# Kernel optimization log

Measured on AMD Instinct MI355X. Metric: run time of the kernel, lower is better.

Reference implementation:

```python
import jax, jax.numpy as jnp
import numpy as np

SIG = 10.0
C = 0.0
STD = 1.0
N_ATOMS = 21
DESC = N_ATOMS * (N_ATOMS - 1) // 2  # 210
N_TRAIN = 4096
M = 128


def setup_inputs() -> dict:
    key = jax.random.key(0)
    k1, k2, k3 = jax.random.split(key, 3)
    # Cartesian coordinates, spread out so interatomic distances are O(1)
    Rs = jax.random.normal(k1, (M, N_ATOMS, 3), dtype=jnp.float32) * 2.0
    # training descriptors are inverse distances -> positive
    xs_train = jax.random.uniform(k2, (N_TRAIN, DESC), dtype=jnp.float32)
    Jx_alphas = jax.random.normal(k3, (N_TRAIN, DESC), dtype=jnp.float32)
    return {"Rs": Rs, "xs_train": xs_train, "Jx_alphas": Jx_alphas}


def reference(Rs, xs_train, Jx_alphas):
    sig, c, std = SIG, C, STD
    n_atoms = Rs.shape[1]
    i, j = np.tril_indices(n_atoms, k=-1)  # static index pattern

    # pairwise displacement vectors, [M, N, N, 3]
    diffs = Rs[:, :, None, :] - Rs[:, None, :, :]
    # gather strict lower triangle first, then take norm (avoids norm-at-zero on diag)
    d_vec = diffs[:, i, j, :]                      # [M, desc, 3]
    r = jnp.linalg.norm(d_vec, axis=-1)            # [M, desc]
    xs = 1.0 / r                                   # inverse-distance descriptor

    q = np.sqrt(5.0) / sig
    # [M, T, desc] broadcast diff vs training descriptors
    x_diffs = (q * xs)[:, None, :] - q * xs_train[None, :, :]
    x_dists = jnp.linalg.norm(x_diffs, axis=-1)    # [M, T]
    exp_xs = (5.0 / (3.0 * sig ** 2)) * jnp.exp(-x_dists)
    dot_x_diff_Jx = jnp.einsum('mtd,td->mt', x_diffs, Jx_alphas)
    exp_xs_1_x_dists = exp_xs * (1.0 + x_dists)

    # force pieces in descriptor space
    F1s_x = jnp.einsum('mt,mtd->md', exp_xs * dot_x_diff_Jx, x_diffs)
    F2s_x = exp_xs_1_x_dists @ Jx_alphas           # [M, desc]
    Fs_x = (F1s_x - F2s_x) * std

    # expand_tril(Fs_x) / dists**3, with zero diagonal (torch sets diag dists=inf)
    coef = Fs_x / r ** 3                           # [M, desc]
    full = jnp.zeros((Rs.shape[0], n_atoms, n_atoms), dtype=Rs.dtype)
    full = full.at[:, i, j].set(coef).at[:, j, i].set(coef)
    # sum over first atom axis (torch dim=1)
    Fs = jnp.einsum('mab,mabc->mbc', full, diffs)  # [M, N, 3]

    Es = jnp.sum(exp_xs_1_x_dists * dot_x_diff_Jx, axis=-1) / q
    Es = c + Es * std
    return Es, Fs
```

## Files before the change

### kernel.cpp

```cpp
#include <hip/hip_runtime.h>
#include <math.h>

#define NATOMS 21
#define DESC 210
#define DPAD 224
#define P4 112
#define NTRAIN 4096
#define NM 128

#define CC 0.0f
#define STDC 1.0f
#define QS 0.22360679774997896f
#define KE 0.016666666666666666f

__device__ __forceinline__ void gll16(const void* gptr, void* lptr) {
    __builtin_amdgcn_global_load_lds(
        (__attribute__((address_space(1))) void*)gptr,
        (__attribute__((address_space(3))) void*)lptr,
        16, 0, 0);
}

__device__ __forceinline__ void pair_ij(int p, int& i, int& j) {
    int ii = (int)((1.0f + sqrtf(1.0f + 8.0f * (float)p)) * 0.5f);
    while (ii * (ii - 1) / 2 > p) --ii;
    while ((ii + 1) * ii / 2 <= p) ++ii;
    i = ii;
    j = p - ii * (ii - 1) / 2;
}

__global__ __launch_bounds__(256, 2) void k_prep(const float* __restrict__ Rs,
                                                 const float* __restrict__ xs_train,
                                                 const float* __restrict__ Jx,
                                                 float2* __restrict__ xj2,
                                                 float* __restrict__ aT,
                                                 float* __restrict__ aPf,
                                                 float* __restrict__ asq,
                                                 float* __restrict__ bsqPart,
                                                 float* __restrict__ cjPart,
                                                 float* __restrict__ Fzero) {
    __shared__ float smem[2 * 32 * 65 + 8];
    const int tid = threadIdx.x;
    const int bid = blockIdx.x;
    {
        const int z = bid * 256 + tid;
        if (z < 2 * 26880) Fzero[z] = 0.0f;
    }
    if (bid < 448) {
        float* ldsX = smem;
        float* ldsJ = smem + 32 * 65;
        const int bx = bid & 63;
        const int by = bid >> 6;
        const int t0 = bx * 64;
        const int d0 = by * 32;
        #pragma unroll
        for (int k = 0; k < 8; ++k) {
            const int idx = tid + k * 256;
            const int tt = idx >> 5;
            const int dd = idx & 31;
            const int d = d0 + dd;
            float xv = 0.0f, jv = 0.0f;
            if (d < DESC) {
                xv = QS * xs_train[(t0 + tt) * DESC + d];
                jv = Jx[(t0 + tt) * DESC + d];
            }
            ldsX[dd * 65 + tt] = xv;
            ldsJ[dd * 65 + tt] = jv;
        }
        __syncthreads();
        #pragma unroll
        for (int k = 0; k < 8; ++k) {
            const int idx = tid + k * 256;
            const int tt = idx >> 5;
            const int dd = idx & 31;
            xj2[(t0 + tt) * 256 + d0 + dd] =
                make_float2(ldsX[dd * 65 + tt], ldsJ[dd * 65 + tt]);
        }
        if (tid < 64) {
            float sb = 0.0f, sc = 0.0f;
            #pragma unroll
            for (int dd = 0; dd < 32; ++dd) {
                const float b = ldsX[dd * 65 + tid];
                const float jj = ldsJ[dd * 65 + tid];
                sb = fmaf(b, b, sb);
                sc = fmaf(b, jj, sc);
            }
            bsqPart[by * NTRAIN + t0 + tid] = sb;
            cjPart[by * NTRAIN + t0 + tid] = sc;
        }
    } else {
        const int m = bid - 448;
        float* R = smem;
        float* red = smem + 64;
        if (tid < NATOMS * 3) R[tid] = Rs[m * NATOMS * 3 + tid];
        __syncthreads();
        float a2 = 0.0f;
        if (tid < DPAD) {
            float a = 0.0f;
            if (tid < DESC) {
                int i, j;
                pair_ij(tid, i, j);
                const float dx = R[i * 3 + 0] - R[j * 3 + 0];
                const float dy = R[i * 3 + 1] - R[j * 3 + 1];
                const float dz = R[i * 3 + 2] - R[j * 3 + 2];
                a = QS / sqrtf(dx * dx + dy * dy + dz * dz);
            }
            aT[tid * NM + m] = a;
            aPf[(tid >> 1) * 256 + m * 2 + (tid & 1)] = a;
            a2 = a * a;
        }
        #pragma unroll
        for (int off = 32; off > 0; off >>= 1) a2 += __shfl_down(a2, off, 64);
        if ((tid & 63) == 0) red[tid >> 6] = a2;
        __syncthreads();
        if (tid == 0) asq[m] = red[0] + red[1] + red[2] + red[3];
    }
}

__global__ __launch_bounds__(256, 4) void k_pass1(const float2* __restrict__ xj2,
                                                  const float2* __restrict__ aP,
                                                  const float* __restrict__ asq,
                                                  const float* __restrict__ bsqPart,
                                                  const float* __restrict__ cjPart,
                                                  float2* __restrict__ w12T,
                                                  float* __restrict__ EsPart,
                                                  float* __restrict__ S1Part) {
    const int tid = threadIdx.x;
    const int bid = blockIdx.x;
    const int ml = tid & 127;
    const int tgu = __builtin_amdgcn_readfirstlane(tid >> 7);
    const int t0 = bid * 4 + tgu * 2;

    float P[2] = {0.f, 0.f};
    float Q[2] = {0.f, 0.f};
    const float2* ap = aP + ml;
    const float4* r0 = (const float4*)(xj2 + (size_t)(t0 + 0) * 256);
    const float4* r1 = (const float4*)(xj2 + (size_t)(t0 + 1) * 256);

    #pragma unroll 8
    for (int p = 0; p < P4; ++p) {
        const float2 a = ap[p * 128];
        const float4 b0 = r0[p];
        const float4 b1 = r1[p];
        P[0] = fmaf(a.x, b0.x, P[0]); P[0] = fmaf(a.y, b0.z, P[0]);
        Q[0] = fmaf(a.x, b0.y, Q[0]); Q[0] = fmaf(a.y, b0.w, Q[0]);
        P[1] = fmaf(a.x, b1.x, P[1]); P[1] = fmaf(a.y, b1.z, P[1]);
        Q[1] = fmaf(a.x, b1.y, Q[1]); Q[1] = fmaf(a.y, b1.w, Q[1]);
    }

    const float asqv = asq[ml];
    float es = 0.f, s1 = 0.f;
    #pragma unroll
    for (int j = 0; j < 2; ++j) {
        const int t = t0 + j;
        float bsqv = 0.f, cjv = 0.f;
        #pragma unroll
        for (int by = 0; by < 7; ++by) {
            bsqv += bsqPart[by * NTRAIN + t];
            cjv += cjPart[by * NTRAIN + t];
        }
        float dist2 = asqv + bsqv - 2.0f * P[j];
        dist2 = fmaxf(dist2, 0.0f);
        const float x = sqrtf(dist2);
        const float e = KE * expf(-x);
        const float dotv = Q[j] - cjv;
        const float w1v = e * dotv;
        const float w2v = e * (1.0f + x);
        w12T[t * NM + ml] = make_float2(w1v, w2v);
        es += w2v * dotv;
        s1 += w1v;
    }
    __shared__ float esL[2][128], s1L[2][128];
    esL[tgu][ml] = es;
    s1L[tgu][ml] = s1;
    __syncthreads();
    if (tid < 128) {
        EsPart[bid * NM + tid] = esL[0][tid] + esL[1][tid];
        S1Part[bid * NM + tid] = s1L[0][tid] + s1L[1][tid];
    }
}

__global__ __launch_bounds__(256, 2) void k_pass2(const float2* __restrict__ xj2,
                                                  const float2* __restrict__ w12T,
                                                  float* __restrict__ F1acc,
                                                  float* __restrict__ F2acc) {
    const int tid = threadIdx.x;
    const int bid = blockIdx.x;
    const int bx = (bid & 7) + 8 * (bid >> 6);
    const int mg = (bid >> 3) & 7;
    const int t0 = bx * 128;
    const int m0 = mg * 16;

    __shared__ __align__(16) float2 wS2[128][16];
    __shared__ __align__(16) float2 xjS[2][8][256];

    #pragma unroll
    for (int k = 0; k < 4; ++k) {
        const int idx = tid + k * 256;
        const int tt = idx >> 3;
        const int f = idx & 7;
        gll16((const float4*)(w12T + (size_t)(t0 + tt) * NM + m0) + f,
              reinterpret_cast<float4*>(wS2) + idx);
    }
    #pragma unroll
    for (int k = 0; k < 4; ++k) {
        const int idx = tid + k * 256;
        const int row = idx >> 7;
        const int col = idx & 127;
        gll16(&xj2[(size_t)(t0 + row) * 256 + 2 * col], &xjS[0][row][2 * col]);
    }

    const int d = (tid < DESC) ? tid : 0;
    float G1[16], G2[16];
    #pragma unroll
    for (int i = 0; i < 16; ++i) { G1[i] = 0.f; G2[i] = 0.f; }

    for (int c = 0; c < 16; ++c) {
        asm volatile("s_waitcnt vmcnt(0) lgkmcnt(0)" ::: "memory");
        __builtin_amdgcn_s_barrier();
        __builtin_amdgcn_sched_barrier(0);
        if (c < 15) {
            float2* dst = &xjS[(c + 1) & 1][0][0];
            #pragma unroll
            for (int k = 0; k < 4; ++k) {
                const int idx = tid + k * 256;
                const int row = idx >> 7;
                const int col = idx & 127;
                gll16(&xj2[(size_t)(t0 + (c + 1) * 8 + row) * 256 + 2 * col],
                      &dst[row * 256 + 2 * col]);
            }
        }
        const float2* xjC = &xjS[c & 1][0][0];
        #pragma unroll
        for (int tt = 0; tt < 8; ++tt) {
            const int tb = c * 8 + tt;
            const float2 xj = xjC[tt * 256 + d];
            const float4* wrow = reinterpret_cast<const float4*>(&wS2[tb][0]);
            #pragma unroll
            for (int k = 0; k < 8; ++k) {
                const float4 w = wrow[k];
                G1[2 * k]     = fmaf(w.x, xj.x, G1[2 * k]);
                G2[2 * k]     = fmaf(w.y, xj.y, G2[2 * k]);
                G1[2 * k + 1] = fmaf(w.z, xj.x, G1[2 * k + 1]);
                G2[2 * k + 1] = fmaf(w.w, xj.y, G2[2 * k + 1]);
            }
        }
    }

    if (tid < DESC) {
        #pragma unroll
        for (int mi = 0; mi < 16; ++mi) {
            atomicAdd(&F1acc[(m0 + mi) * DESC + tid], G1[mi]);
            atomicAdd(&F2acc[(m0 + mi) * DESC + tid], G2[mi]);
        }
    }
}

__global__ __launch_bounds__(256) void k_final(const float* __restrict__ Rs,
                                               const float* __restrict__ aT,
                                               const float* __restrict__ EsPart,
                                               const float* __restrict__ S1Part,
                                               const float* __restrict__ F1acc,
                                               const float* __restrict__ F2acc,
                                               float* __restrict__ out) {
    const int m = blockIdx.x;
    __shared__ float R[NATOMS * 3];
    __shared__ float FsL[NATOMS * 3];
    __shared__ float redE[4], redS[4];
    __shared__ float sEs, sS1;
    const int tid = threadIdx.x;
    float esp = 0.f, s1p = 0.f;
    #pragma unroll
    for (int k = 0; k < 4; ++k) {
        esp += EsPart[(tid + k * 256) * NM + m];
        s1p += S1Part[(tid + k * 256) * NM + m];
    }
    #pragma unroll
    for (int off = 32; off > 0; off >>= 1) {
        esp += __shfl_down(esp, off, 64);
        s1p += __shfl_down(s1p, off, 64);
    }
    if ((tid & 63) == 0) { redE[tid >> 6] = esp; redS[tid >> 6] = s1p; }
    if (tid < NATOMS * 3) {
        R[tid] = Rs[m * NATOMS * 3 + tid];
        FsL[tid] = 0.0f;
    }
    __syncthreads();
    if (tid == 0) {
        sEs = redE[0] + redE[1] + redE[2] + redE[3];
        sS1 = redS[0] + redS[1] + redS[2] + redS[3];
    }
    __syncthreads();
    if (tid < DESC) {
        int i, j;
        pair_ij(tid, i, j);
        const float dx = R[i * 3 + 0] - R[j * 3 + 0];
        const float dy = R[i * 3 + 1] - R[j * 3 + 1];
        const float dz = R[i * 3 + 2] - R[j * 3 + 2];
        const float r2 = dx * dx + dy * dy + dz * dz;
        const float rinv = 1.0f / sqrtf(r2);
        const float a = aT[tid * NM + m];
        const float F1 = a * sS1 - F1acc[m * DESC + tid];
        const float Fx = (F1 - F2acc[m * DESC + tid]) * STDC;
        const float coef = Fx * (rinv * rinv * rinv);
        atomicAdd(&FsL[j * 3 + 0], coef * dx);
        atomicAdd(&FsL[j * 3 + 1], coef * dy);
        atomicAdd(&FsL[j * 3 + 2], coef * dz);
        atomicAdd(&FsL[i * 3 + 0], -coef * dx);
        atomicAdd(&FsL[i * 3 + 1], -coef * dy);
        atomicAdd(&FsL[i * 3 + 2], -coef * dz);
    }
    __syncthreads();
    if (tid < NATOMS * 3) out[NM + m * NATOMS * 3 + tid] = FsL[tid];
    if (tid == 0) out[m] = CC + (sEs / QS) * STDC;
}

extern "C" void kernel_launch(void* const* d_in, const int* in_sizes, int n_in,
                              void* d_out, int out_size, void* d_ws, size_t ws_size,
                              hipStream_t stream) {
    const float* Rs = (const float*)d_in[0];
    const float* xs_train = (const float*)d_in[1];
    const float* Jx = (const float*)d_in[2];
    float* out = (float*)d_out;
    float* ws = (float*)d_ws;

    float* F1acc = ws;
    float* F2acc = ws + 26880;
    float* bsqPart = ws + 53760;
    float* cjPart = ws + 82432;
    float* aT = ws + 111104;
    float* asq = ws + 139776;
    float* aPf = ws + 139904;
    float* EsPart = ws + 168576;
    float* S1Part = ws + 299648;
    float2* w12T = (float2*)(ws + 430720);
    float2* xj2 = (float2*)(ws + 1479296);

    k_prep<<<576, 256, 0, stream>>>(Rs, xs_train, Jx, xj2, aT, aPf, asq,
                                    bsqPart, cjPart, F1acc);
    k_pass1<<<1024, 256, 0, stream>>>(xj2, (const float2*)aPf, asq, bsqPart, cjPart,
                                      w12T, EsPart, S1Part);
    k_pass2<<<256, 256, 0, stream>>>(xj2, w12T, F1acc, F2acc);
    k_final<<<NM, 256, 0, stream>>>(Rs, aT, EsPart, S1Part, F1acc, F2acc, out);
}
```

Before: 71.96 us.

## Triple-buffer pass2 xj loads and halve per-block train chunk to double grid

The pass2 kernel now covers 64 training rows per block instead of 128 and launches 512 blocks instead of 256, which raises parallelism across the CUs. The xj staging in LDS moves from double to triple buffering with a prefetch distance of two chunks, and a partial vmcnt wait lets the next chunk's loads stay in flight during compute. The cost is twice as many atomicAdds into F1acc/F2acc, since there are twice as many blocks, plus somewhat more LDS per block.

New measurement: 104.0 us. 44.5% more time.

```diff
diff --git a/kernel.cpp b/kernel.cpp
--- a/kernel.cpp
+++ b/kernel.cpp
@@ -187,26 +187,29 @@
     const int bid = blockIdx.x;
     const int bx = (bid & 7) + 8 * (bid >> 6);
     const int mg = (bid >> 3) & 7;
-    const int t0 = bx * 128;
+    const int t0 = bx * 64;
     const int m0 = mg * 16;
 
-    __shared__ __align__(16) float2 wS2[128][16];
-    __shared__ __align__(16) float2 xjS[2][8][256];
-
-    #pragma unroll
-    for (int k = 0; k < 4; ++k) {
-        const int idx = tid + k * 256;
-        const int tt = idx >> 3;
-        const int f = idx & 7;
-        gll16((const float4*)(w12T + (size_t)(t0 + tt) * NM + m0) + f,
-              reinterpret_cast<float4*>(wS2) + idx);
-    }
-    #pragma unroll
-    for (int k = 0; k < 4; ++k) {
-        const int idx = tid + k * 256;
-        const int row = idx >> 7;
-        const int col = idx & 127;
-        gll16(&xj2[(size_t)(t0 + row) * 256 + 2 * col], &xjS[0][row][2 * col]);
+    __shared__ __align__(16) float2 wS2[64][16];
+    __shared__ __align__(16) float2 xjS[3][8][256];
+
+    {
+        #pragma unroll
+        for (int k = 0; k < 2; ++k) {
+            const int idx = tid + k * 256;
+            gll16((const float4*)(w12T + (size_t)(t0 + (idx >> 3)) * NM + m0) + (idx & 7),
+                  reinterpret_cast<float4*>(wS2) + idx);
+        }
+        const int row = tid >> 7;
+        const int col = tid & 127;
+        #pragma unroll
+        for (int k = 0; k < 4; ++k)
+            gll16(&xj2[(size_t)(t0 + row + 2 * k) * 256 + 2 * col],
+                  &xjS[0][row + 2 * k][2 * col]);
+        #pragma unroll
+        for (int k = 0; k < 4; ++k)
+            gll16(&xj2[(size_t)(t0 + 8 + row + 2 * k) * 256 + 2 * col],
+                  &xjS[1][row + 2 * k][2 * col]);
     }
 
     const int d = (tid < DESC) ? tid : 0;
@@ -214,22 +217,15 @@
     #pragma unroll
     for (int i = 0; i < 16; ++i) { G1[i] = 0.f; G2[i] = 0.f; }
 
-    for (int c = 0; c < 16; ++c) {
-        asm volatile("s_waitcnt vmcnt(0) lgkmcnt(0)" ::: "memory");
+    for (int c = 0; c < 8; ++c) {
+        if (c < 7) {
+            asm volatile("s_waitcnt vmcnt(4) lgkmcnt(0)" ::: "memory");
+        } else {
+            asm volatile("s_waitcnt vmcnt(0) lgkmcnt(0)" ::: "memory");
+        }
         __builtin_amdgcn_s_barrier();
         __builtin_amdgcn_sched_barrier(0);
-        if (c < 15) {
-            float2* dst = &xjS[(c + 1) & 1][0][0];
-            #pragma unroll
-            for (int k = 0; k < 4; ++k) {
-                const int idx = tid + k * 256;
-                const int row = idx >> 7;
-                const int col = idx & 127;
-                gll16(&xj2[(size_t)(t0 + (c + 1) * 8 + row) * 256 + 2 * col],
-                      &dst[row * 256 + 2 * col]);
-            }
-        }
-        const float2* xjC = &xjS[c & 1][0][0];
+        const float2* xjC = &xjS[c % 3][0][0];
         #pragma unroll
         for (int tt = 0; tt < 8; ++tt) {
             const int tb = c * 8 + tt;
@@ -243,6 +239,15 @@
                 G1[2 * k + 1] = fmaf(w.z, xj.x, G1[2 * k + 1]);
                 G2[2 * k + 1] = fmaf(w.w, xj.y, G2[2 * k + 1]);
             }
+        }
+        if (c < 6) {
+            const int row = tid >> 7;
+            const int col = tid & 127;
+            float2* dst = &xjS[(c + 2) % 3][0][0];
+            #pragma unroll
+            for (int k = 0; k < 4; ++k)
+                gll16(&xj2[(size_t)(t0 + (c + 2) * 8 + row + 2 * k) * 256 + 2 * col],
+                      &dst[(row + 2 * k) * 256 + 2 * col]);
         }
     }
 
@@ -339,6 +344,6 @@
                                     bsqPart, cjPart, F1acc);
     k_pass1<<<1024, 256, 0, stream>>>(xj2, (const float2*)aPf, asq, bsqPart, cjPart,
                                       w12T, EsPart, S1Part);
-    k_pass2<<<256, 256, 0, stream>>>(xj2, w12T, F1acc, F2acc);
+    k_pass2<<<512, 256, 0, stream>>>(xj2, w12T, F1acc, F2acc);
     k_final<<<NM, 256, 0, stream>>>(Rs, aT, EsPart, S1Part, F1acc, F2acc, out);
 }
```
